# Performance work log

Measured on AMD Instinct MI355X. Metric: run time of the kernel, lower is better.

The kernel has to match this reference:

```python
import jax, jax.numpy as jnp
import numpy as np

H = 512   # hidden_size
L = 20    # num_labels
B, S = 32, 256


def _uniform(key, shape, k):
    return jax.random.uniform(key, shape, minval=-k, maxval=k, dtype=jnp.float32)


def setup_inputs() -> dict:
    key = jax.random.key(0)
    ks = iter(jax.random.split(key, 40))
    k = 1.0 / np.sqrt(H)
    inp = {
        "inputs": jax.random.normal(next(ks), (B, S, H), dtype=jnp.float32),
        "labels": jax.random.randint(next(ks), (B, S), 0, L),
        "mask": jnp.ones((B, S), dtype=jnp.int32),
    }
    for layer, din in ((0, H), (1, 2 * H)):
        for d in ("f", "b"):
            inp[f"w_ih_l{layer}{d}"] = _uniform(next(ks), (4 * H, din), k)
            inp[f"w_hh_l{layer}{d}"] = _uniform(next(ks), (4 * H, H), k)
            inp[f"b_ih_l{layer}{d}"] = _uniform(next(ks), (4 * H,), k)
            inp[f"b_hh_l{layer}{d}"] = _uniform(next(ks), (4 * H,), k)
    kf = 1.0 / np.sqrt(2 * H)
    inp["fc_w"] = _uniform(next(ks), (L, 2 * H), kf)
    inp["fc_b"] = _uniform(next(ks), (L,), kf)
    inp["trans_m"] = jax.random.normal(next(ks), (L, L), dtype=jnp.float32) * 0.1
    inp["start_scores"] = jax.random.normal(next(ks), (L,), dtype=jnp.float32) * 0.1
    inp["end_scores"] = jax.random.normal(next(ks), (L,), dtype=jnp.float32) * 0.1
    return inp


def _lstm_dir(x, wih, whh, bih, bhh, reverse):
    # x: [S, B, Din] -> hs: [S, B, H] (outputs in original time order)
    _, b, _ = x.shape
    hh = whh.shape[1]
    xw = jnp.einsum('sbd,gd->sbg', x, wih) + bih + bhh  # precompute input projections

    def step(carry, xt):
        h, c = carry
        g = xt + h @ whh.T  # [B, 4H]
        i, f, gg, o = jnp.split(g, 4, axis=-1)  # pytorch gate order i,f,g,o
        c = jax.nn.sigmoid(f) * c + jax.nn.sigmoid(i) * jnp.tanh(gg)
        h = jax.nn.sigmoid(o) * jnp.tanh(c)
        return (h, c), h

    init = (jnp.zeros((b, hh), x.dtype), jnp.zeros((b, hh), x.dtype))
    _, hs = jax.lax.scan(step, init, xw, reverse=reverse)
    return hs


def _crf_loss(logits, tags, maskf, trans, start, end):
    # logits [S,B,L], tags [S,B], maskf [S,B] float. Returns per-sample NLL [B].
    s, b, n = logits.shape
    # --- normalizer (forward algorithm) ---
    alpha0 = logits[0] + start  # [B, n]

    def step(alpha, inp):
        emit, m = inp  # emit [B,n], m [B]
        tmp = alpha[:, :, None] + trans[None, :, :] + emit[:, None, :]  # [B, from, to]
        new = jax.nn.logsumexp(tmp, axis=1)
        alpha = jnp.where(m[:, None] > 0, new, alpha)
        return alpha, None

    alpha, _ = jax.lax.scan(step, alpha0, (logits[1:], maskf[1:]))
    norm = jax.nn.logsumexp(alpha + end, axis=1)  # [B]
    # --- gold path score ---
    emit = jnp.take_along_axis(logits, tags[:, :, None], axis=2)[:, :, 0] * maskf  # [S,B]
    trans_sc = trans[tags[:-1], tags[1:]] * maskf[1:]  # [S-1,B]
    last_idx = maskf.sum(0).astype(jnp.int32) - 1  # [B]
    last_tags = tags[last_idx, jnp.arange(b)]
    gold = emit.sum(0) + trans_sc.sum(0) + start[tags[0]] + end[last_tags]
    return norm - gold


def reference(inputs, labels, mask,
              w_ih_l0f, w_hh_l0f, b_ih_l0f, b_hh_l0f,
              w_ih_l0b, w_hh_l0b, b_ih_l0b, b_hh_l0b,
              w_ih_l1f, w_hh_l1f, b_ih_l1f, b_hh_l1f,
              w_ih_l1b, w_hh_l1b, b_ih_l1b, b_hh_l1b,
              fc_w, fc_b, trans_m, start_scores, end_scores):
    x = jnp.transpose(inputs, (1, 0, 2))  # [S,B,H]
    h0 = jnp.concatenate([
        _lstm_dir(x, w_ih_l0f, w_hh_l0f, b_ih_l0f, b_hh_l0f, False),
        _lstm_dir(x, w_ih_l0b, w_hh_l0b, b_ih_l0b, b_hh_l0b, True),
    ], axis=-1)  # [S,B,2H]
    h1 = jnp.concatenate([
        _lstm_dir(h0, w_ih_l1f, w_hh_l1f, b_ih_l1f, b_hh_l1f, False),
        _lstm_dir(h0, w_ih_l1b, w_hh_l1b, b_ih_l1b, b_hh_l1b, True),
    ], axis=-1)  # [S,B,2H]
    logits = h1 @ fc_w.T + fc_b  # [S,B,L]
    tags = labels.T  # [S,B]
    maskf = mask.T.astype(logits.dtype)
    loss = _crf_loss(logits, tags, maskf, trans_m, start_scores, end_scores)
    return loss.mean()
```

## Files before the change

kernel.cpp:

```cpp
#include <hip/hip_runtime.h>

#define Sx 256
#define Bx 32
#define Hx 512
#define Gx 2048
#define Lx 20
#define Rx 8192

typedef __attribute__((ext_vector_type(8))) short short8;
typedef __attribute__((ext_vector_type(4))) float f32x4;
typedef __attribute__((ext_vector_type(16))) float f32x16;

__device__ __forceinline__ unsigned short f2bf(float f) {
  union { float f; unsigned u; } v; v.f = f;
  unsigned u = v.u;
  return (unsigned short)((u + 0x7fffu + ((u >> 16) & 1u)) >> 16);
}
__device__ __forceinline__ float bf2f(unsigned short h) {
  union { unsigned u; float f; } v; v.u = ((unsigned)h) << 16;
  return v.f;
}
__device__ __forceinline__ float bfh(unsigned long long x, int r) {
  return bf2f((unsigned short)((x >> (16 * r)) & 0xffffull));
}
__device__ __forceinline__ float sigmf(float x) { return 1.0f / (1.0f + expf(-x)); }

__device__ __forceinline__ float fsigm(float x) {
  return __builtin_amdgcn_rcpf(1.0f + __builtin_amdgcn_exp2f(-1.44269504f * x));
}
__device__ __forceinline__ float ftanh(float x) {
  return __builtin_fmaf(-2.0f,
      __builtin_amdgcn_rcpf(1.0f + __builtin_amdgcn_exp2f(2.88539008f * x)), 1.0f);
}
#define L2E 1.44269504088896f
#define LN2 0.69314718055995f


__global__ void k_pack_x(const float* __restrict__ x, unsigned short* __restrict__ xbf) {
  int tid = blockIdx.x * 256 + threadIdx.x;
  int h = tid & (Hx - 1);
  int r = tid >> 9;
  int b = r & 31;
  int t = r >> 5;
  xbf[tid] = f2bf(x[(b * Sx + t) * Hx + h]);
}

__global__ void k_cast(const float* __restrict__ s, unsigned short* __restrict__ d, int n) {
  int i = blockIdx.x * 256 + threadIdx.x;
  if (i < n) d[i] = f2bf(s[i]);
}

__global__ void k_add2(const float* __restrict__ a, const float* __restrict__ b,
                       float* __restrict__ o, int n) {
  int i = blockIdx.x * 256 + threadIdx.x;
  if (i < n) o[i] = a[i] + b[i];
}

__global__ void k_repack(const unsigned short* __restrict__ hT, unsigned short* __restrict__ rows) {
  int tid = blockIdx.x * 256 + threadIdx.x;
  int b = tid & 31;
  int kt = (tid >> 5) & 63;
  int t = (tid >> 11) & 255;
  int dir = tid >> 19;
  short8 v = *(const short8*)&hT[(size_t)tid * 8];
  *(short8*)&rows[((size_t)(t * 32 + b)) * 1024 + dir * 512 + kt * 8] = v;
}

__global__ __launch_bounds__(256) void k_gemm(
    const unsigned short* __restrict__ A,
    const unsigned short* __restrict__ Bw,
    const float* __restrict__ bias,
    unsigned short* __restrict__ C,
    int M, int N, int K)
{
  const int bn = blockIdx.x, bm = blockIdx.y;
  const int tid = threadIdx.x;
  const int w = tid >> 6, lane = tid & 63;
  const int wr = w >> 1, wc = w & 1;
  const int lo = lane & 15, qd = lane >> 4;

  __shared__ unsigned short As[128 * 72];
  __shared__ unsigned short Bs[128 * 72];

  f32x4 acc[4][4] = {};

  const int ktn = K >> 6;
  for (int kt = 0; kt < ktn; ++kt) {
    __syncthreads();
#pragma unroll
    for (int p = 0; p < 4; ++p) {
      int c = tid + (p << 8);
      int row = c >> 3, kc = c & 7;
      *(short8*)&As[row * 72 + kc * 8] =
          *(const short8*)&A[(size_t)(bm * 128 + row) * K + kt * 64 + kc * 8];
      *(short8*)&Bs[row * 72 + kc * 8] =
          *(const short8*)&Bw[(size_t)(bn * 128 + row) * K + kt * 64 + kc * 8];
    }
    __syncthreads();
#pragma unroll
    for (int kk = 0; kk < 2; ++kk) {
      short8 af[4], bfr[4];
#pragma unroll
      for (int mi = 0; mi < 4; ++mi)
        af[mi] = *(const short8*)&As[(wr * 64 + mi * 16 + lo) * 72 + kk * 32 + qd * 8];
#pragma unroll
      for (int ni = 0; ni < 4; ++ni)
        bfr[ni] = *(const short8*)&Bs[(wc * 64 + ni * 16 + lo) * 72 + kk * 32 + qd * 8];
#pragma unroll
      for (int mi = 0; mi < 4; ++mi)
#pragma unroll
        for (int ni = 0; ni < 4; ++ni)
          acc[mi][ni] = __builtin_amdgcn_mfma_f32_16x16x32_bf16(af[mi], bfr[ni], acc[mi][ni], 0, 0, 0);
    }
  }
#pragma unroll
  for (int mi = 0; mi < 4; ++mi) {
#pragma unroll
    for (int ni = 0; ni < 4; ++ni) {
      int n = bn * 128 + wc * 64 + ni * 16 + lo;
      float bv = bias[n];
      int wsb = (n >> 4) & 31, cg = n >> 9, jl = n & 15;
      size_t base = (size_t)wsb * (Rx * 64) + (size_t)cg * 16 + jl;
#pragma unroll
      for (int r = 0; r < 4; ++r) {
        int m = bm * 128 + wr * 64 + mi * 16 + qd * 4 + r;
        C[base + (size_t)m * 64] = f2bf(acc[mi][ni][r] + bv);
      }
    }
  }
}

__global__ __launch_bounds__(256, 1) void k_lstm(
    const unsigned short* __restrict__ xwF,
    const unsigned short* __restrict__ xwB,
    const unsigned short* __restrict__ whF,
    const unsigned short* __restrict__ whB,
    unsigned short* __restrict__ hT,
    unsigned int* __restrict__ flags,
    unsigned int* __restrict__ done)
{
  const int wg = blockIdx.x;
  const int tid = threadIdx.x;

  __shared__ unsigned short Ws[64 * 512];

  if (wg >= 64) {
    asm volatile("s_setprio 0");
    float a = 1.0f + (float)tid, bm = 1.0000001f, cm = 1.0e-7f;
    for (;;) {
#pragma unroll 8
      for (int i = 0; i < 512; ++i) a = __builtin_fmaf(a, bm, cm);
      if (__hip_atomic_load(done, __ATOMIC_RELAXED, __HIP_MEMORY_SCOPE_AGENT) >= 64u) break;
    }
    if (a == 123.456789f) ((volatile float*)hT)[0] = a;
    return;
  }

  asm volatile("s_setprio 3");
  const int dir = wg >> 5;
  const int vs = wg & 31;
  const int j0 = vs * 16;
  const unsigned short* xw = (dir ? xwB : xwF) + (size_t)vs * (Rx * 64);
  const unsigned short* wh = dir ? whB : whF;
  unsigned short* hTd = hT + (size_t)dir * (Sx * 16384);
  unsigned int* fl = flags + dir * 32 * 32;

  {
    const int l6 = tid & 63;
#pragma unroll
    for (int i = 0; i < 16; ++i) {
      int rr = (tid >> 6) * 16 + i;
      int g = ((rr >> 4) << 9) + j0 + (rr & 15);
      int pc = l6 ^ (rr & 7);
      *(short8*)&Ws[rr * 512 + pc * 8] = *(const short8*)&wh[(size_t)g * Hx + l6 * 8];
    }
  }
  __syncthreads();
  if (tid >= 64) return;

  const int lane = tid;
  const int bn = lane & 31;
  const int q  = lane >> 5;

  float cst[2][4] = {};

  for (int s = 0; s < Sx; ++s) {
    const int t = dir ? (Sx - 1 - s) : s;

    const unsigned short* xwt = xw + ((size_t)t * 32 + bn) * 64 + q * 4;
    unsigned long long xg[4][2];
#pragma unroll
    for (int c = 0; c < 4; ++c)
#pragma unroll
      for (int jg = 0; jg < 2; ++jg)
        xg[c][jg] = *(const unsigned long long*)(xwt + c * 16 + jg * 8);
    __asm__ __volatile__("" ::: "memory");

    f32x16 acc0, acc1;

    if (s > 0) {
      const unsigned tgt = (unsigned)s;
      const int tp = dir ? (t + 1) : (t - 1);
      const unsigned short* hb = hTd + (size_t)tp * 16384 + lane * 8;

      short8 hreg[32];
      unsigned v0 = __hip_atomic_load(fl + (lane & 31) * 32,
                                      __ATOMIC_RELAXED, __HIP_MEMORY_SCOPE_AGENT);
#pragma unroll
      for (int ks = 0; ks < 32; ++ks)
        hreg[ks] = *(const short8*)(hb + ks * 512);
#pragma unroll
      for (int ks = 0; ks < 32; ++ks)
        asm volatile("" :: "v"(hreg[ks]));
      if (!__all((int)(v0 >= tgt))) {
        unsigned v;
        do {
          __asm__ __volatile__("" ::: "memory");
          v = __hip_atomic_load(fl + (lane & 31) * 32,
                                __ATOMIC_RELAXED, __HIP_MEMORY_SCOPE_AGENT);
        } while (!__all((int)(v >= tgt)));
        __asm__ __volatile__("" ::: "memory");
#pragma unroll
        for (int ks = 0; ks < 32; ++ks)
          hreg[ks] = *(const short8*)(hb + ks * 512);
#pragma unroll
        for (int ks = 0; ks < 32; ++ks)
          asm volatile("" :: "v"(hreg[ks]));
      }
      __builtin_amdgcn_sched_barrier(0);

      f32x16 a0 = {}, a1 = {}, b0 = {}, b1 = {};
#pragma unroll
      for (int ks = 0; ks < 32; ks += 2) {
        int lc0 = ks * 2 + q, lc1 = (ks + 1) * 2 + q;
        int pc0 = lc0 ^ (bn & 7), pc1 = lc1 ^ (bn & 7);
        short8 af00 = *(const short8*)&Ws[bn * 512 + pc0 * 8];
        short8 af10 = *(const short8*)&Ws[(32 + bn) * 512 + pc0 * 8];
        short8 af01 = *(const short8*)&Ws[bn * 512 + pc1 * 8];
        short8 af11 = *(const short8*)&Ws[(32 + bn) * 512 + pc1 * 8];
        a0 = __builtin_amdgcn_mfma_f32_32x32x16_bf16(af00, hreg[ks],     a0, 0, 0, 0);
        a1 = __builtin_amdgcn_mfma_f32_32x32x16_bf16(af10, hreg[ks],     a1, 0, 0, 0);
        b0 = __builtin_amdgcn_mfma_f32_32x32x16_bf16(af01, hreg[ks + 1], b0, 0, 0, 0);
        b1 = __builtin_amdgcn_mfma_f32_32x32x16_bf16(af11, hreg[ks + 1], b1, 0, 0, 0);
      }
      acc0 = a0 + b0;
      acc1 = a1 + b1;
    } else {
      acc0 = (f32x16){};
      acc1 = (f32x16){};
    }

#pragma unroll
    for (int jg = 0; jg < 2; ++jg) {
      unsigned long long hv = 0;
#pragma unroll
      for (int r = 0; r < 4; ++r) {
        float iv = acc0[jg * 4 + r]     + bfh(xg[0][jg], r);
        float fv = acc0[8 + jg * 4 + r] + bfh(xg[1][jg], r);
        float gv = acc1[jg * 4 + r]     + bfh(xg[2][jg], r);
        float ov = acc1[8 + jg * 4 + r] + bfh(xg[3][jg], r);
        float ct = fsigm(fv) * cst[jg][r] + fsigm(iv) * ftanh(gv);
        cst[jg][r] = ct;
        float hvf = fsigm(ov) * ftanh(ct);
        hv |= (unsigned long long)f2bf(hvf) << (16 * r);
      }
      unsigned short* hw = hTd + (size_t)t * 16384 + ((size_t)(vs * 2 + jg) * 32 + bn) * 8 + q * 4;
      __hip_atomic_store((unsigned long long*)hw, hv,
                         __ATOMIC_RELAXED, __HIP_MEMORY_SCOPE_AGENT);
    }

    __asm__ __volatile__("s_waitcnt vmcnt(0)" ::: "memory");
    if (lane == 0)
      __hip_atomic_store(fl + vs * 32, (unsigned)(s + 1),
                         __ATOMIC_RELAXED, __HIP_MEMORY_SCOPE_AGENT);
  }

  if (lane == 0)
    __hip_atomic_fetch_add(done, 1u, __ATOMIC_RELAXED, __HIP_MEMORY_SCOPE_AGENT);
}

__global__ __launch_bounds__(256) void k_fc(
    const unsigned short* __restrict__ h1T,
    const float* __restrict__ fcw,
    const float* __restrict__ fcb,
    float* __restrict__ logits)
{
  int row = blockIdx.x;
  int t = row >> 5, b = row & 31;
  int l = threadIdx.x & 31;
  int sl = threadIdx.x >> 5;
  __shared__ float red[8][32];
  float p = 0.f;
  if (l < Lx) {
#pragma unroll 4
    for (int kt = sl * 16; kt < sl * 16 + 16; ++kt) {
      int k = kt * 8;
      int dir = k >> 9, kk = k & 511;
      const unsigned short* hp = h1T + (size_t)dir * (Sx * 16384) + (size_t)t * 16384
                                 + ((size_t)(kk >> 3) * 32 + b) * 8;
      short8 hv = *(const short8*)hp;
      const float* wr = fcw + l * 1024 + k;
      f32x4 w0 = *(const f32x4*)wr;
      f32x4 w1 = *(const f32x4*)(wr + 4);
      p += bf2f((unsigned short)hv[0]) * w0[0] + bf2f((unsigned short)hv[1]) * w0[1]
         + bf2f((unsigned short)hv[2]) * w0[2] + bf2f((unsigned short)hv[3]) * w0[3]
         + bf2f((unsigned short)hv[4]) * w1[0] + bf2f((unsigned short)hv[5]) * w1[1]
         + bf2f((unsigned short)hv[6]) * w1[2] + bf2f((unsigned short)hv[7]) * w1[3];
    }
  }
  red[sl][l] = p;
  __syncthreads();
  if (threadIdx.x < Lx) {
    float s = fcb[threadIdx.x];
#pragma unroll
    for (int i = 0; i < 8; ++i) s += red[i][threadIdx.x];
    logits[(size_t)row * Lx + threadIdx.x] = s;
  }
}

__global__ __launch_bounds__(64) void k_crf(
    const float* __restrict__ logits,
    const int* __restrict__ labels,
    const int* __restrict__ mask,
    const float* __restrict__ trans,
    const float* __restrict__ startv,
    const float* __restrict__ endv,
    float* __restrict__ out)
{
  int b = blockIdx.x;
  int tid = threadIdx.x;
  __shared__ float tr[Lx * Lx];
  __shared__ float al[2][Lx];
  __shared__ float norm_s;
  for (int i = tid; i < Lx * Lx; i += 64) tr[i] = trans[i];
  if (tid < Lx) al[0][tid] = logits[b * Lx + tid] + startv[tid];
  __syncthreads();
  int cur = 0;
  float em = (tid < Lx) ? logits[((size_t)1 * Bx + b) * Lx + tid] : 0.f;
  int m = mask[b * Sx + 1];
  for (int t = 1; t < Sx; ++t) {
    float em_next = 0.f;
    int m_next = 0;
    if (t + 1 < Sx) {
      if (tid < Lx) em_next = logits[((size_t)(t + 1) * Bx + b) * Lx + tid];
      m_next = mask[b * Sx + t + 1];
    }
    if (tid < Lx) {
      int to = tid;
      float v[Lx];
      float mx = -1e30f;
#pragma unroll
      for (int f = 0; f < Lx; ++f) { v[f] = al[cur][f] + tr[f * Lx + to]; mx = fmaxf(mx, v[f]); }
      float sum = 0.f;
#pragma unroll
      for (int f = 0; f < Lx; ++f) sum += __builtin_amdgcn_exp2f((v[f] - mx) * L2E);
      float nv = mx + LN2 * __builtin_amdgcn_logf(sum) + em;
      al[1 - cur][to] = (m > 0) ? nv : al[cur][to];
    }
    __syncthreads();
    cur ^= 1;
    em = em_next;
    m = m_next;
  }
  if (tid == 0) {
    float mx = -1e30f;
    for (int l = 0; l < Lx; ++l) mx = fmaxf(mx, al[cur][l] + endv[l]);
    float s = 0.f;
    for (int l = 0; l < Lx; ++l) s += __builtin_amdgcn_exp2f((al[cur][l] + endv[l] - mx) * L2E);
    norm_s = mx + LN2 * __builtin_amdgcn_logf(s);
  }
  __syncthreads();
  const int* lab = labels + b * Sx;
  const int* msk = mask + b * Sx;
  float part = 0.f;
  int msum = 0;
  for (int t = tid; t < Sx; t += 64) {
    int mm = msk[t];
    int tg = lab[t];
    if (mm > 0) {
      part += logits[((size_t)t * Bx + b) * Lx + tg];
      if (t >= 1) part += tr[lab[t - 1] * Lx + tg];
      msum++;
    }
  }
#pragma unroll
  for (int o = 32; o > 0; o >>= 1) {
    part += __shfl_down(part, o, 64);
    msum += __shfl_down(msum, o, 64);
  }
  if (tid == 0) {
    float gold = part + startv[lab[0]] + endv[lab[msum - 1]];
    atomicAdd(out, (norm_s - gold) * (1.0f / 32.0f));
  }
}


extern "C" void kernel_launch(void* const* d_in, const int* in_sizes, int n_in,
                              void* d_out, int out_size, void* d_ws, size_t ws_size,
                              hipStream_t stream)
{
  const float* x      = (const float*)d_in[0];
  const int* labels   = (const int*)d_in[1];
  const int* mask     = (const int*)d_in[2];
  const float* wih0f  = (const float*)d_in[3];
  const float* whh0f  = (const float*)d_in[4];
  const float* bih0f  = (const float*)d_in[5];
  const float* bhh0f  = (const float*)d_in[6];
  const float* wih0b  = (const float*)d_in[7];
  const float* whh0b  = (const float*)d_in[8];
  const float* bih0b  = (const float*)d_in[9];
  const float* bhh0b  = (const float*)d_in[10];
  const float* wih1f  = (const float*)d_in[11];
  const float* whh1f  = (const float*)d_in[12];
  const float* bih1f  = (const float*)d_in[13];
  const float* bhh1f  = (const float*)d_in[14];
  const float* wih1b  = (const float*)d_in[15];
  const float* whh1b  = (const float*)d_in[16];
  const float* bih1b  = (const float*)d_in[17];
  const float* bhh1b  = (const float*)d_in[18];
  const float* fcw    = (const float*)d_in[19];
  const float* fcb    = (const float*)d_in[20];
  const float* transm = (const float*)d_in[21];
  const float* startv = (const float*)d_in[22];
  const float* endv   = (const float*)d_in[23];

  char* p = (char*)d_ws;
  auto alloc = [&](size_t bytes) -> char* {
    char* r = p;
    p += (bytes + 255) & ~((size_t)255);
    return r;
  };

  unsigned short* x_bf    = (unsigned short*)alloc((size_t)Rx * Hx * 2);
  unsigned short* wih0f_b = (unsigned short*)alloc((size_t)Gx * Hx * 2);
  unsigned short* wih0b_b = (unsigned short*)alloc((size_t)Gx * Hx * 2);
  unsigned short* whh0f_b = (unsigned short*)alloc((size_t)Gx * Hx * 2);
  unsigned short* whh0b_b = (unsigned short*)alloc((size_t)Gx * Hx * 2);
  unsigned short* wih1f_b = (unsigned short*)alloc((size_t)Gx * 1024 * 2);
  unsigned short* wih1b_b = (unsigned short*)alloc((size_t)Gx * 1024 * 2);
  unsigned short* whh1f_b = (unsigned short*)alloc((size_t)Gx * Hx * 2);
  unsigned short* whh1b_b = (unsigned short*)alloc((size_t)Gx * Hx * 2);
  float* bias0f = (float*)alloc(Gx * 4);
  float* bias0b = (float*)alloc(Gx * 4);
  float* bias1f = (float*)alloc(Gx * 4);
  float* bias1b = (float*)alloc(Gx * 4);
  unsigned short* xw_f = (unsigned short*)alloc((size_t)Rx * Gx * 2);
  unsigned short* xw_b = (unsigned short*)alloc((size_t)Rx * Gx * 2);
  unsigned short* h0T  = (unsigned short*)alloc((size_t)2 * Sx * 16384 * 2);
  unsigned short* h1T  = (unsigned short*)alloc((size_t)2 * Sx * 16384 * 2);
  unsigned short* h0rows = (unsigned short*)alloc((size_t)Rx * 1024 * 2);
  float* logits = (float*)alloc((size_t)Rx * Lx * 4);
  unsigned int* flagsA = (unsigned int*)alloc(2 * 32 * 32 * 4);
  unsigned int* flagsB = (unsigned int*)alloc(2 * 32 * 32 * 4);
  unsigned int* doneA  = (unsigned int*)alloc(256);
  unsigned int* doneB  = (unsigned int*)alloc(256);

  if ((size_t)(p - (char*)d_ws) > ws_size) return;

  hipMemsetAsync(flagsA, 0, 2 * 32 * 32 * 4, stream);
  hipMemsetAsync(flagsB, 0, 2 * 32 * 32 * 4, stream);
  hipMemsetAsync(doneA, 0, 256, stream);
  hipMemsetAsync(doneB, 0, 256, stream);

  k_pack_x<<<(Rx * Hx) / 256, 256, 0, stream>>>(x, x_bf);
  k_cast<<<(Gx * Hx) / 256, 256, 0, stream>>>(wih0f, wih0f_b, Gx * Hx);
  k_cast<<<(Gx * Hx) / 256, 256, 0, stream>>>(wih0b, wih0b_b, Gx * Hx);
  k_cast<<<(Gx * Hx) / 256, 256, 0, stream>>>(whh0f, whh0f_b, Gx * Hx);
  k_cast<<<(Gx * Hx) / 256, 256, 0, stream>>>(whh0b, whh0b_b, Gx * Hx);
  k_cast<<<(Gx * 1024) / 256, 256, 0, stream>>>(wih1f, wih1f_b, Gx * 1024);
  k_cast<<<(Gx * 1024) / 256, 256, 0, stream>>>(wih1b, wih1b_b, Gx * 1024);
  k_cast<<<(Gx * Hx) / 256, 256, 0, stream>>>(whh1f, whh1f_b, Gx * Hx);
  k_cast<<<(Gx * Hx) / 256, 256, 0, stream>>>(whh1b, whh1b_b, Gx * Hx);
  k_add2<<<Gx / 256, 256, 0, stream>>>(bih0f, bhh0f, bias0f, Gx);
  k_add2<<<Gx / 256, 256, 0, stream>>>(bih0b, bhh0b, bias0b, Gx);
  k_add2<<<Gx / 256, 256, 0, stream>>>(bih1f, bhh1f, bias1f, Gx);
  k_add2<<<Gx / 256, 256, 0, stream>>>(bih1b, bhh1b, bias1b, Gx);

  k_gemm<<<dim3(Gx / 128, Rx / 128), 256, 0, stream>>>(x_bf, wih0f_b, bias0f, xw_f, Rx, Gx, Hx);
  k_gemm<<<dim3(Gx / 128, Rx / 128), 256, 0, stream>>>(x_bf, wih0b_b, bias0b, xw_b, Rx, Gx, Hx);
  k_lstm<<<256, 256, 0, stream>>>(xw_f, xw_b, whh0f_b, whh0b_b, h0T, flagsA, doneA);

  k_repack<<<4096, 256, 0, stream>>>(h0T, h0rows);

  k_gemm<<<dim3(Gx / 128, Rx / 128), 256, 0, stream>>>(h0rows, wih1f_b, bias1f, xw_f, Rx, Gx, 1024);
  k_gemm<<<dim3(Gx / 128, Rx / 128), 256, 0, stream>>>(h0rows, wih1b_b, bias1b, xw_b, Rx, Gx, 1024);
  k_lstm<<<256, 256, 0, stream>>>(xw_f, xw_b, whh1f_b, whh1b_b, h1T, flagsB, doneB);

  k_fc<<<Rx, 256, 0, stream>>>(h1T, fcw, fcb, logits);
  hipMemsetAsync(d_out, 0, 4, stream);
  k_crf<<<Bx, 64, 0, stream>>>(logits, labels, mask, transm, startv, endv, (float*)d_out);
}
```

Before: 2.613 ms.

## Replace per-step flag handshake with poisoned hidden-state polling in LSTM

Drops the per-workgroup step flags and the vmcnt drain plus flag store after each timestep. Consumers instead poll the hidden-state buffer itself, which is pre-filled with a poison bf16 pattern, and spin until no loaded value equals the poison. This removes one round trip (store data, wait, store flag, consumer reads flag, then reads data) from the serial recurrence critical path. In exchange, the h buffers must be memset each call, and the code relies on each 8-byte atomic store being seen whole and on no real h value equalling 0x7F7F. Only the first halfword of each 8-byte word is checked.

Result: slower. 2.923 ms (+11.9%).

```diff
diff --git a/kernel.cpp b/kernel.cpp
--- a/kernel.cpp
+++ b/kernel.cpp
@@ -34,6 +34,8 @@
 }
 #define L2E 1.44269504088896f
 #define LN2 0.69314718055995f
+
+#define POISON16 0x7F7Fu
 
 
 __global__ void k_pack_x(const float* __restrict__ x, unsigned short* __restrict__ xbf) {
@@ -136,7 +138,6 @@
     const unsigned short* __restrict__ whF,
     const unsigned short* __restrict__ whB,
     unsigned short* __restrict__ hT,
-    unsigned int* __restrict__ flags,
     unsigned int* __restrict__ done)
 {
   const int wg = blockIdx.x;
@@ -163,7 +164,6 @@
   const unsigned short* xw = (dir ? xwB : xwF) + (size_t)vs * (Rx * 64);
   const unsigned short* wh = dir ? whB : whF;
   unsigned short* hTd = hT + (size_t)dir * (Sx * 16384);
-  unsigned int* fl = flags + dir * 32 * 32;
 
   {
     const int l6 = tid & 63;
@@ -199,35 +199,34 @@
     f32x16 acc0, acc1;
 
     if (s > 0) {
-      const unsigned tgt = (unsigned)s;
       const int tp = dir ? (t + 1) : (t - 1);
       const unsigned short* hb = hTd + (size_t)tp * 16384 + lane * 8;
 
-      short8 hreg[32];
-      unsigned v0 = __hip_atomic_load(fl + (lane & 31) * 32,
+      unsigned long long hu0[32], hu1[32];
+      for (;;) {
+#pragma unroll
+        for (int ks = 0; ks < 32; ++ks) {
+          hu0[ks] = __hip_atomic_load((const unsigned long long*)(hb + ks * 512),
                                       __ATOMIC_RELAXED, __HIP_MEMORY_SCOPE_AGENT);
-#pragma unroll
-      for (int ks = 0; ks < 32; ++ks)
-        hreg[ks] = *(const short8*)(hb + ks * 512);
-#pragma unroll
-      for (int ks = 0; ks < 32; ++ks)
-        asm volatile("" :: "v"(hreg[ks]));
-      if (!__all((int)(v0 >= tgt))) {
-        unsigned v;
-        do {
-          __asm__ __volatile__("" ::: "memory");
-          v = __hip_atomic_load(fl + (lane & 31) * 32,
-                                __ATOMIC_RELAXED, __HIP_MEMORY_SCOPE_AGENT);
-        } while (!__all((int)(v >= tgt)));
-        __asm__ __volatile__("" ::: "memory");
+          hu1[ks] = __hip_atomic_load((const unsigned long long*)(hb + ks * 512 + 4),
+                                      __ATOMIC_RELAXED, __HIP_MEMORY_SCOPE_AGENT);
+        }
+        int ok = 1;
 #pragma unroll
         for (int ks = 0; ks < 32; ++ks)
-          hreg[ks] = *(const short8*)(hb + ks * 512);
-#pragma unroll
-        for (int ks = 0; ks < 32; ++ks)
-          asm volatile("" :: "v"(hreg[ks]));
+          ok &= ((unsigned short)hu0[ks] != POISON16) & ((unsigned short)hu1[ks] != POISON16);
+        if (__all(ok)) break;
       }
       __builtin_amdgcn_sched_barrier(0);
+
+      short8 hreg[32];
+#pragma unroll
+      for (int ks = 0; ks < 32; ++ks) {
+        union { unsigned long long u[2]; short8 v; } cv;
+        cv.u[0] = hu0[ks];
+        cv.u[1] = hu1[ks];
+        hreg[ks] = cv.v;
+      }
 
       f32x16 a0 = {}, a1 = {}, b0 = {}, b1 = {};
 #pragma unroll
@@ -268,11 +267,6 @@
       __hip_atomic_store((unsigned long long*)hw, hv,
                          __ATOMIC_RELAXED, __HIP_MEMORY_SCOPE_AGENT);
     }
-
-    __asm__ __volatile__("s_waitcnt vmcnt(0)" ::: "memory");
-    if (lane == 0)
-      __hip_atomic_store(fl + vs * 32, (unsigned)(s + 1),
-                         __ATOMIC_RELAXED, __HIP_MEMORY_SCOPE_AGENT);
   }
 
   if (lane == 0)
@@ -450,15 +444,13 @@
   unsigned short* h1T  = (unsigned short*)alloc((size_t)2 * Sx * 16384 * 2);
   unsigned short* h0rows = (unsigned short*)alloc((size_t)Rx * 1024 * 2);
   float* logits = (float*)alloc((size_t)Rx * Lx * 4);
-  unsigned int* flagsA = (unsigned int*)alloc(2 * 32 * 32 * 4);
-  unsigned int* flagsB = (unsigned int*)alloc(2 * 32 * 32 * 4);
   unsigned int* doneA  = (unsigned int*)alloc(256);
   unsigned int* doneB  = (unsigned int*)alloc(256);
 
   if ((size_t)(p - (char*)d_ws) > ws_size) return;
 
-  hipMemsetAsync(flagsA, 0, 2 * 32 * 32 * 4, stream);
-  hipMemsetAsync(flagsB, 0, 2 * 32 * 32 * 4, stream);
+  hipMemsetAsync(h0T, 0x7F, (size_t)2 * Sx * 16384 * 2, stream);
+  hipMemsetAsync(h1T, 0x7F, (size_t)2 * Sx * 16384 * 2, stream);
   hipMemsetAsync(doneA, 0, 256, stream);
   hipMemsetAsync(doneB, 0, 256, stream);
 
@@ -478,13 +470,13 @@
 
   k_gemm<<<dim3(Gx / 128, Rx / 128), 256, 0, stream>>>(x_bf, wih0f_b, bias0f, xw_f, Rx, Gx, Hx);
   k_gemm<<<dim3(Gx / 128, Rx / 128), 256, 0, stream>>>(x_bf, wih0b_b, bias0b, xw_b, Rx, Gx, Hx);
-  k_lstm<<<256, 256, 0, stream>>>(xw_f, xw_b, whh0f_b, whh0b_b, h0T, flagsA, doneA);
+  k_lstm<<<256, 256, 0, stream>>>(xw_f, xw_b, whh0f_b, whh0b_b, h0T, doneA);
 
   k_repack<<<4096, 256, 0, stream>>>(h0T, h0rows);
 
   k_gemm<<<dim3(Gx / 128, Rx / 128), 256, 0, stream>>>(h0rows, wih1f_b, bias1f, xw_f, Rx, Gx, 1024);
   k_gemm<<<dim3(Gx / 128, Rx / 128), 256, 0, stream>>>(h0rows, wih1b_b, bias1b, xw_b, Rx, Gx, 1024);
-  k_lstm<<<256, 256, 0, stream>>>(xw_f, xw_b, whh1f_b, whh1b_b, h1T, flagsB, doneB);
+  k_lstm<<<256, 256, 0, stream>>>(xw_f, xw_b, whh1f_b, whh1b_b, h1T, doneB);
 
   k_fc<<<Rx, 256, 0, stream>>>(h1T, fcw, fcb, logits);
   hipMemsetAsync(d_out, 0, 4, stream);
```
